# Performance work log

Hardware: AMD Instinct MI355X
Metric: run time of the kernel (lower is better)

The kernel has to match this reference:

```python
import jax, jax.numpy as jnp
import numpy as np

B, S, H, NH, HD = 2, 2048, 1024, 16, 64
RD = 16            # rotary_dim = head_dim * 0.25
W = 16             # mini_context_length (sliding window)
SCALE = HD ** -0.5
ROPE_BASE = 10000.0


def setup_inputs() -> dict:
    key = jax.random.key(0)
    ks = jax.random.split(key, 10)
    p = lambda k, shape: (jax.random.normal(k, shape, dtype=jnp.float32) * 0.02)
    return {
        "hidden_states": jax.random.normal(ks[0], (B, S, H), dtype=jnp.float32),
        "Wqkv": p(ks[1], (3 * H, H)), "bqkv": p(ks[2], (3 * H,)),
        "Wqa": p(ks[3], (H, H)),      "bqa": p(ks[4], (H,)),
        "Wka": p(ks[5], (H, H)),      "bka": p(ks[6], (H,)),
        "Wd": p(ks[7], (H, H)),       "bd": p(ks[8], (H,)),
    }


def _rotate_half(x):
    x1, x2 = jnp.split(x, 2, axis=-1)
    return jnp.concatenate([-x2, x1], axis=-1)


def _apply_rope(q, k, seq_len):
    # GPT-NeoX style rotary on the first RD dims. q,k: [B,NH,S,RD]
    inv_freq = 1.0 / (ROPE_BASE ** (jnp.arange(0, RD, 2, dtype=jnp.float32) / RD))
    t = jnp.arange(seq_len, dtype=jnp.float32)
    freqs = jnp.outer(t, inv_freq)                     # [S, RD//2]
    emb = jnp.concatenate([freqs, freqs], axis=-1)     # [S, RD]
    cos = jnp.cos(emb)[None, None]                      # [1,1,S,RD]
    sin = jnp.sin(emb)[None, None]
    return q * cos + _rotate_half(q) * sin, k * cos + _rotate_half(k) * sin


def reference(hidden_states, Wqkv, bqkv, Wqa, bqa, Wka, bka, Wd, bd):
    b, s, _ = hidden_states.shape
    qkv = hidden_states @ Wqkv.T + bqkv                       # [B,S,3H]
    qkv = qkv.reshape(b, s, 3, NH, HD).transpose(2, 0, 3, 1, 4)
    q, k, v = qkv[0], qkv[1], qkv[2]                          # [B,NH,S,HD]

    q_rot, k_rot = _apply_rope(q[..., :RD], k[..., :RD], s)
    q = jnp.concatenate([q_rot, q[..., RD:]], axis=-1)
    k = jnp.concatenate([k_rot, k[..., RD:]], axis=-1)

    # ----- Stage 1: sliding-window local attention (vectorized) -----
    pos = jnp.arange(s)
    idx = pos[:, None] - (W - 1) + jnp.arange(W)[None, :]     # [S,W]
    valid = idx >= 0
    idxc = jnp.clip(idx, 0, s - 1)
    k_win = k[:, :, idxc, :]                                   # [B,NH,S,W,HD]
    v_win = v[:, :, idxc, :]
    scores = jnp.einsum('bhsd,bhswd->bhsw', q, k_win) * SCALE
    scores = jnp.where(valid[None, None], scores, -jnp.inf)
    probs = jax.nn.softmax(scores, axis=-1)
    A = jnp.einsum('bhsw,bhswd->bhsd', probs, v_win)           # [B,NH,S,HD]

    A_hidden = A.transpose(0, 2, 1, 3).reshape(b, s, H)        # [B,S,H]

    # ----- Stage 2: causal global attention over A -----
    qa = (A_hidden @ Wqa.T + bqa).reshape(b, s, NH, HD).transpose(0, 2, 1, 3)
    ka = (A_hidden @ Wka.T + bka).reshape(b, s, NH, HD).transpose(0, 2, 1, 3)
    g = jnp.einsum('bhqd,bhkd->bhqk', qa, ka) * SCALE          # [B,NH,S,S]
    causal = pos[:, None] >= pos[None, :]
    g = jnp.where(causal[None, None], g, -jnp.inf)
    pg = jax.nn.softmax(g, axis=-1)
    out = jnp.einsum('bhqk,bhkd->bhqd', pg, A)                 # [B,NH,S,HD]
    out = out.transpose(0, 2, 1, 3).reshape(b, s, H)
    return out @ Wd.T + bd
```

## Files before the change

kernel.cpp:

```cpp
#include <hip/hip_runtime.h>
#include <hip/hip_bf16.h>
#include <cstdint>
#include <cstddef>

typedef __bf16 bf16;
typedef __bf16 bf16x4 __attribute__((ext_vector_type(4)));
typedef __bf16 bf16x8 __attribute__((ext_vector_type(8)));
typedef float  f32x4  __attribute__((ext_vector_type(4)));

#define DEVINL __device__ __forceinline__

constexpr int   Bc  = 2, Sc = 2048, Hc = 1024, NHc = 16, HDc = 64;
constexpr int   Tc  = Bc * Sc;
constexpr float L2E = 1.44269504088896340736f;
constexpr float NEG_BIG = -1.0e30f;

typedef __attribute__((address_space(1))) void AS1void;
typedef __attribute__((address_space(3))) void AS3void;

DEVINL void load_lds16(const bf16* g, bf16* l) {
  __builtin_amdgcn_global_load_lds((AS1void*)g, (AS3void*)l, 16, 0, 0);
}


__global__ __launch_bounds__(256)
void convert_all(const float* __restrict__ hs, const float* __restrict__ Wqkv,
                 const float* __restrict__ Wqa, const float* __restrict__ Wka,
                 const float* __restrict__ Wd, const float* __restrict__ bqa,
                 const float* __restrict__ bka,
                 bf16* __restrict__ hsb, bf16* __restrict__ wqkvb,
                 bf16* __restrict__ wqakab, bf16* __restrict__ wdb,
                 float* __restrict__ bqaka) {
  const int blk = blockIdx.x;
  if (blk >= 5120) {
    const int i = threadIdx.x * 8;
    const float* src = (i < 1024) ? (bqa + i) : (bka + i - 1024);
    *(f32x4*)(bqaka + i)     = *(const f32x4*)src;
    *(f32x4*)(bqaka + i + 4) = *(const f32x4*)(src + 4);
    return;
  }
  const float* src; bf16* dst; int base;
  if      (blk < 2048) { src = hs;   dst = hsb;                    base = blk; }
  else if (blk < 3584) { src = Wqkv; dst = wqkvb;                  base = blk - 2048; }
  else if (blk < 4096) { src = Wqa;  dst = wqakab;                 base = blk - 3584; }
  else if (blk < 4608) { src = Wka;  dst = wqakab + 1024 * 1024;   base = blk - 4096; }
  else                 { src = Wd;   dst = wdb;                    base = blk - 4608; }
  const int i = (base * 256 + threadIdx.x) * 8;
  f32x4 a = *(const f32x4*)(src + i);
  f32x4 b = *(const f32x4*)(src + i + 4);
  bf16x8 v;
#pragma unroll
  for (int j = 0; j < 4; j++) { v[j] = (bf16)a[j]; v[4 + j] = (bf16)b[j]; }
  *(bf16x8*)(dst + i) = v;
}

template <typename CT>
__global__ __launch_bounds__(256, 2)
void gemm128(const bf16* __restrict__ A, const bf16* __restrict__ Bw,
             const float* __restrict__ bias, CT* __restrict__ C,
             int M, int N, int K) {
  __shared__ __attribute__((aligned(16))) bf16 As[128 * 64];
  __shared__ __attribute__((aligned(16))) bf16 Bs[128 * 64];

  const int tid = threadIdx.x, wv = tid >> 6, lane = tid & 63;
  const int m0 = blockIdx.y * 128, n0 = blockIdx.x * 128;
  const int col = lane & 15, quad = lane >> 4;
  const int wrow = (wv >> 1) * 64, wcol = (wv & 1) * 64;

  f32x4 acc[4][4];
#pragma unroll
  for (int i = 0; i < 4; i++)
#pragma unroll
    for (int j = 0; j < 4; j++) acc[i][j] = f32x4{0.f, 0.f, 0.f, 0.f};

  const int srow = tid >> 3;
  const int scol = (((tid & 7) ^ (srow & 7)) << 3);
  const bf16* Ag = A  + (size_t)(m0 + srow) * K + scol;
  const bf16* Bg = Bw + (size_t)(n0 + srow) * K + scol;
  const int cs = col & 7;

  for (int k0 = 0; k0 < K; k0 += 64) {
#pragma unroll
    for (int c = 0; c < 4; c++) {
      load_lds16(Ag + (size_t)(c * 32) * K + k0, As + c * 2048 + tid * 8);
      load_lds16(Bg + (size_t)(c * 32) * K + k0, Bs + c * 2048 + tid * 8);
    }
    __syncthreads();
#pragma unroll
    for (int kk = 0; kk < 64; kk += 32) {
      const int so = ((((kk >> 3) + quad) ^ cs) << 3);
      bf16x8 af[4], bfr[4];
#pragma unroll
      for (int i = 0; i < 4; i++)
        af[i] = *(const bf16x8*)(As + (wrow + i * 16 + col) * 64 + so);
#pragma unroll
      for (int j = 0; j < 4; j++)
        bfr[j] = *(const bf16x8*)(Bs + (wcol + j * 16 + col) * 64 + so);
#pragma unroll
      for (int i = 0; i < 4; i++)
#pragma unroll
        for (int j = 0; j < 4; j++)
          acc[i][j] = __builtin_amdgcn_mfma_f32_16x16x32_bf16(af[i], bfr[j], acc[i][j], 0, 0, 0);
    }
    __syncthreads();
  }

#pragma unroll
  for (int j = 0; j < 4; j++) {
    const int c = n0 + wcol + j * 16 + col;
    const float bv = bias[c];
#pragma unroll
    for (int i = 0; i < 4; i++)
#pragma unroll
      for (int r = 0; r < 4; r++) {
        const int rr = m0 + wrow + i * 16 + quad * 4 + r;
        C[(size_t)rr * N + c] = (CT)(acc[i][j][r] + bv);
      }
  }
}

template <typename CT>
__global__ __launch_bounds__(256, 2)
void gemm64(const bf16* __restrict__ A, const bf16* __restrict__ Bw,
            const float* __restrict__ bias, CT* __restrict__ C,
            int M, int N, int K) {
  __shared__ __attribute__((aligned(16))) bf16 As[64 * 64];
  __shared__ __attribute__((aligned(16))) bf16 Bs[128 * 64];

  const int tid = threadIdx.x, wv = tid >> 6, lane = tid & 63;
  const int m0 = blockIdx.y * 64, n0 = blockIdx.x * 128;
  const int col = lane & 15, quad = lane >> 4;
  const int wrow = (wv >> 1) * 32, wcol = (wv & 1) * 64;

  f32x4 acc[2][4];
#pragma unroll
  for (int i = 0; i < 2; i++)
#pragma unroll
    for (int j = 0; j < 4; j++) acc[i][j] = f32x4{0.f, 0.f, 0.f, 0.f};

  const int srow = tid >> 3;
  const int scol = (((tid & 7) ^ (srow & 7)) << 3);
  const bf16* Ag = A  + (size_t)(m0 + srow) * K + scol;
  const bf16* Bg = Bw + (size_t)(n0 + srow) * K + scol;
  const int cs = col & 7;

  for (int k0 = 0; k0 < K; k0 += 64) {
#pragma unroll
    for (int c = 0; c < 2; c++)
      load_lds16(Ag + (size_t)(c * 32) * K + k0, As + c * 2048 + tid * 8);
#pragma unroll
    for (int c = 0; c < 4; c++)
      load_lds16(Bg + (size_t)(c * 32) * K + k0, Bs + c * 2048 + tid * 8);
    __syncthreads();
#pragma unroll
    for (int kk = 0; kk < 64; kk += 32) {
      const int so = ((((kk >> 3) + quad) ^ cs) << 3);
      bf16x8 af[2], bfr[4];
#pragma unroll
      for (int i = 0; i < 2; i++)
        af[i] = *(const bf16x8*)(As + (wrow + i * 16 + col) * 64 + so);
#pragma unroll
      for (int j = 0; j < 4; j++)
        bfr[j] = *(const bf16x8*)(Bs + (wcol + j * 16 + col) * 64 + so);
#pragma unroll
      for (int i = 0; i < 2; i++)
#pragma unroll
        for (int j = 0; j < 4; j++)
          acc[i][j] = __builtin_amdgcn_mfma_f32_16x16x32_bf16(af[i], bfr[j], acc[i][j], 0, 0, 0);
    }
    __syncthreads();
  }

#pragma unroll
  for (int j = 0; j < 4; j++) {
    const int c = n0 + wcol + j * 16 + col;
    const float bv = bias[c];
#pragma unroll
    for (int i = 0; i < 2; i++)
#pragma unroll
      for (int r = 0; r < 4; r++) {
        const int rr = m0 + wrow + i * 16 + quad * 4 + r;
        C[(size_t)rr * N + c] = (CT)(acc[i][j][r] + bv);
      }
  }
}

__global__ __launch_bounds__(256)
void window_attn(const bf16* __restrict__ qkv, bf16* __restrict__ Ah,
                 bf16* __restrict__ VTg) {
  __shared__ __attribute__((aligned(16))) bf16 Kw[31 * 72];
  __shared__ __attribute__((aligned(16))) bf16 Vw[31 * 72];
  const int g  = blockIdx.x;
  const int st = g & 127;
  const int h  = (g >> 7) & 15;
  const int b  = g >> 11;
  const int s0 = st * 16;
  const int tid = threadIdx.x;

  if ((tid < 124) || (tid >= 128 && tid < 252)) {
    const bool isK = tid < 124;
    const int lt  = isK ? tid : tid - 128;
    const int r   = lt >> 2, off = (lt & 3) << 4;
    int sidx = s0 - 15 + r; if (sidx < 0) sidx = 0;
    const bf16* src = qkv + (size_t)(b * Sc + sidx) * 3072 + (isK ? 1024 : 2048) + h * 64 + off;
    bf16x8 v0 = *(const bf16x8*)src;
    bf16x8 v1 = *(const bf16x8*)(src + 8);
    if (isK && off == 0) {
#pragma unroll
      for (int j = 0; j < 8; j++) {
        const float invf = exp2f(-(float)j * 1.66096404744368128f);
        float sn, csn;
        sincosf((float)sidx * invf, &sn, &csn);
        const float x1 = (float)v0[j], x2 = (float)v1[j];
        v0[j] = (bf16)(x1 * csn - x2 * sn);
        v1[j] = (bf16)(x2 * csn + x1 * sn);
      }
    }
    bf16* dst = (isK ? Kw : Vw) + r * 72 + off;
    *(bf16x8*)dst       = v0;
    *(bf16x8*)(dst + 8) = v1;
  }
  __syncthreads();

  const int wv = tid >> 6, lane = tid & 63;
  const int subq = lane >> 4, lane16 = lane & 15;
  const int s = s0 + wv * 4 + subq;
  const int t = b * Sc + s;
  const int d0 = lane16 * 4;

  float qd[4];
  {
    bf16x4 qv = *(const bf16x4*)(qkv + (size_t)t * 3072 + h * 64 + d0);
#pragma unroll
    for (int j = 0; j < 4; j++) qd[j] = (float)qv[j];
  }
  float pd[4];
#pragma unroll
  for (int j = 0; j < 4; j++) pd[j] = __shfl_xor(qd[j], 2, 64);
  if (lane16 < 4) {
#pragma unroll
    for (int j = 0; j < 4; j++) {
      const int jabs = d0 + j;
      const float invf = exp2f(-(float)(jabs & 7) * 1.66096404744368128f);
      float sn, csn;
      sincosf((float)s * invf, &sn, &csn);
      qd[j] = (jabs < 8) ? (qd[j] * csn - pd[j] * sn) : (qd[j] * csn + pd[j] * sn);
    }
  }

  float sc[16];
#pragma unroll
  for (int w = 0; w < 16; w++) {
    const int idxp = s - 15 + w;
    const int row = idxp - s0 + 15;
    bf16x4 kv = *(const bf16x4*)(Kw + row * 72 + d0);
    float p = qd[0] * (float)kv[0] + qd[1] * (float)kv[1] +
              qd[2] * (float)kv[2] + qd[3] * (float)kv[3];
#pragma unroll
    for (int m = 1; m < 16; m <<= 1) p += __shfl_xor(p, m, 64);
    sc[w] = (idxp < 0) ? NEG_BIG : p * 0.125f;
  }
  float mx = sc[0];
#pragma unroll
  for (int w = 1; w < 16; w++) mx = fmaxf(mx, sc[w]);
  float sum = 0.f;
#pragma unroll
  for (int w = 0; w < 16; w++) { sc[w] = exp2f((sc[w] - mx) * L2E); sum += sc[w]; }
  const float inv = 1.0f / fmaxf(sum, 1e-30f);

  float acc[4] = {0.f, 0.f, 0.f, 0.f};
#pragma unroll
  for (int w = 0; w < 16; w++) {
    const int idxp = s - 15 + w;
    const int row = idxp - s0 + 15;
    bf16x4 vv = *(const bf16x4*)(Vw + row * 72 + d0);
#pragma unroll
    for (int j = 0; j < 4; j++) acc[j] += sc[w] * (float)vv[j];
  }
  bf16x4 ov;
#pragma unroll
  for (int j = 0; j < 4; j++) ov[j] = (bf16)(acc[j] * inv);
  *(bf16x4*)(Ah + (size_t)t * 1024 + h * 64 + d0) = ov;
  bf16* vt = VTg + (((size_t)(b * 16 + h)) * 64 + d0) * 2048 + s;
#pragma unroll
  for (int j = 0; j < 4; j++) vt[(size_t)j * 2048] = ov[j];
}

__global__ __launch_bounds__(256, 2)
void flash_attn(const bf16* __restrict__ Q, const bf16* __restrict__ Kt,
                const bf16* __restrict__ VTg, bf16* __restrict__ O) {
  constexpr int QS = 2048;
  constexpr float SHIFT = 16.0f;
  __shared__ __attribute__((aligned(16))) bf16 K_lds[128 * 64];
  __shared__ __attribute__((aligned(16))) bf16 VT_lds[64 * 128];
  __shared__ __attribute__((aligned(16))) bf16 P_lds[4][16 * 136];

  const int tid = threadIdx.x, wv = tid >> 6, lane = tid & 63;
  const int bh = blockIdx.x;
  const int pr = blockIdx.y;
  const int b = bh >> 4, h = bh & 15;
  const int col = lane & 15, quad = lane >> 4;
  const size_t bS = (size_t)b * Sc;
  const int hd = h * 64;

  const int krow = tid >> 3;
  const int kcol = (((tid & 7) ^ (krow & 7)) << 3);
  const int vrow = tid >> 4;
  const int vcol = (((tid & 15) ^ vrow) << 3);
  const int cs8 = col & 7;

  for (int ph = 0; ph < 2; ph++) {
    const int qt = (ph == 0) ? pr : 31 - pr;
    const int qbase = qt * 64 + wv * 16;
    const int nkt = (qt + 2) >> 1;

    const bf16* qptr = Q + (bS + qbase + col) * QS + hd + quad * 8;
    bf16x8 qf[2];
    qf[0] = *(const bf16x8*)qptr;
    qf[1] = *(const bf16x8*)(qptr + 32);
#pragma unroll
    for (int hh = 0; hh < 2; hh++)
#pragma unroll
      for (int j = 0; j < 8; j++) qf[hh][j] = (bf16)((float)qf[hh][j] * 0.125f);

    f32x4 oacc[4];
#pragma unroll
    for (int i = 0; i < 4; i++) oacc[i] = f32x4{0.f, 0.f, 0.f, 0.f};
    float lrow[4] = {0.f, 0.f, 0.f, 0.f};

    for (int kt0 = 0; kt0 < nkt; kt0++) {
      const int k0 = kt0 * 128;
#pragma unroll
      for (int c = 0; c < 4; c++) {
        load_lds16(Kt + (bS + k0 + c * 32 + krow) * QS + hd + kcol,
                   K_lds + c * 2048 + tid * 8);
        load_lds16(VTg + ((size_t)bh * 64 + c * 16 + vrow) * 2048 + k0 + vcol,
                   VT_lds + c * 2048 + tid * 8);
      }
      __syncthreads();

      f32x4 sacc[8];
#pragma unroll
      for (int sub = 0; sub < 8; sub++) {
        f32x4 a = f32x4{0.f, 0.f, 0.f, 0.f};
#pragma unroll
        for (int hh = 0; hh < 2; hh++) {
          const int so = (((hh * 4 + quad) ^ cs8) << 3);
          bf16x8 kf = *(const bf16x8*)(K_lds + (sub * 16 + col) * 64 + so);
          a = __builtin_amdgcn_mfma_f32_16x16x32_bf16(qf[hh], kf, a, 0, 0, 0);
        }
        sacc[sub] = a;
      }
      if (kt0 == nkt - 1) {
#pragma unroll
        for (int sub = 0; sub < 8; sub++)
#pragma unroll
          for (int r = 0; r < 4; r++) {
            const int key = k0 + sub * 16 + col;
            const int qq  = qbase + quad * 4 + r;
            if (key > qq) sacc[sub][r] = NEG_BIG;
          }
      }
#pragma unroll
      for (int sub = 0; sub < 8; sub++)
#pragma unroll
        for (int r = 0; r < 4; r++)
          sacc[sub][r] = exp2f(sacc[sub][r] * L2E - SHIFT);
#pragma unroll
      for (int r = 0; r < 4; r++)
        lrow[r] += ((sacc[0][r] + sacc[1][r]) + (sacc[2][r] + sacc[3][r]))
                 + ((sacc[4][r] + sacc[5][r]) + (sacc[6][r] + sacc[7][r]));
#pragma unroll
      for (int sub = 0; sub < 8; sub++)
#pragma unroll
        for (int r = 0; r < 4; r++)
          P_lds[wv][(quad * 4 + r) * 136 + sub * 16 + col] = (bf16)sacc[sub][r];
#pragma unroll
      for (int kk = 0; kk < 128; kk += 32) {
        bf16x8 pf = *(const bf16x8*)&P_lds[wv][col * 136 + kk + quad * 8];
        const int vso = ((((kk >> 3) + quad) ^ col) << 3);
#pragma unroll
        for (int nb = 0; nb < 4; nb++) {
          bf16x8 vf = *(const bf16x8*)(VT_lds + (nb * 16 + col) * 128 + vso);
          oacc[nb] = __builtin_amdgcn_mfma_f32_16x16x32_bf16(pf, vf, oacc[nb], 0, 0, 0);
        }
      }
      __syncthreads();
    }

#pragma unroll
    for (int m = 1; m < 16; m <<= 1)
#pragma unroll
      for (int r = 0; r < 4; r++) lrow[r] += __shfl_xor(lrow[r], m, 64);
#pragma unroll
    for (int r = 0; r < 4; r++) lrow[r] = 1.0f / fmaxf(lrow[r], 1e-37f);
#pragma unroll
    for (int nb = 0; nb < 4; nb++)
#pragma unroll
      for (int r = 0; r < 4; r++) {
        const int qq = qbase + quad * 4 + r;
        O[(bS + qq) * 1024 + hd + nb * 16 + col] = (bf16)(oacc[nb][r] * lrow[r]);
      }
  }
}

extern "C" void kernel_launch(void* const* d_in, const int* in_sizes, int n_in,
                              void* d_out, int out_size, void* d_ws, size_t ws_size,
                              hipStream_t stream) {
  (void)in_sizes; (void)n_in; (void)out_size; (void)ws_size;
  const float* hs   = (const float*)d_in[0];
  const float* Wqkv = (const float*)d_in[1];
  const float* bqkv = (const float*)d_in[2];
  const float* Wqa  = (const float*)d_in[3];
  const float* bqa  = (const float*)d_in[4];
  const float* Wka  = (const float*)d_in[5];
  const float* bka  = (const float*)d_in[6];
  const float* Wd   = (const float*)d_in[7];
  const float* bd   = (const float*)d_in[8];
  float* out = (float*)d_out;

  const size_t TH = (size_t)Tc * Hc;
  bf16* dob   = (bf16*)d_out;
  bf16* hsb   = dob;
  bf16* wqkvb = dob + TH;
  bf16* Ah    = dob;
  bf16* VTg   = dob + TH;
  bf16* ws     = (bf16*)d_ws;
  bf16* qkv    = ws;
  bf16* qaka   = ws;
  bf16* oh     = ws + 2 * TH;
  bf16* wqakab = ws + 3 * TH;
  bf16* wdb    = wqakab + 2 * 1024 * 1024;
  float* bqaka = (float*)(wdb + 1024 * 1024);

  convert_all<<<dim3(5121), 256, 0, stream>>>(hs, Wqkv, Wqa, Wka, Wd, bqa, bka,
                                              hsb, wqkvb, wqakab, wdb, bqaka);

  gemm128<bf16><<<dim3(24, 32), 256, 0, stream>>>(hsb, wqkvb, bqkv, qkv, Tc, 3 * Hc, Hc);
  window_attn<<<dim3(Tc * NHc / 16), 256, 0, stream>>>(qkv, Ah, VTg);
  gemm128<bf16><<<dim3(16, 32), 256, 0, stream>>>(Ah, wqakab, bqaka, qaka, Tc, 2 * Hc, Hc);
  flash_attn<<<dim3(Bc * NHc, 16), 256, 0, stream>>>(qaka, qaka + Hc, VTg, oh);
  gemm64<float><<<dim3(8, 64), 256, 0, stream>>>(oh, wdb, bd, out, Tc, Hc, Hc);
}
```

Measured before the change: 234.2 us.

## Split flash-attn q-tile pairs into separate blocks, shrink output GEMM tile, raise occupancy

The flash attention kernel no longer loops over a paired short and long query tile inside one block. Each block now handles a single query tile, which doubles the grid to 32 tiles per head, and tiles are ordered in interleaved groups to spread causal work across the launch. The final projection GEMM moves to a 64x64 tile, giving twice as many blocks with one MFMA row per wave. Launch-bounds occupancy hints are raised on the GEMMs and flash kernel. The aim is better GPU fill and latency hiding, at the cost of less per-block work balancing, less data reuse in the smaller GEMM tile, and possible register pressure from the higher occupancy targets.

```diff
diff --git a/kernel.cpp b/kernel.cpp
--- a/kernel.cpp
+++ b/kernel.cpp
@@ -55,7 +55,7 @@
 }
 
 template <typename CT>
-__global__ __launch_bounds__(256, 2)
+__global__ __launch_bounds__(256, 3)
 void gemm128(const bf16* __restrict__ A, const bf16* __restrict__ Bw,
              const float* __restrict__ bias, CT* __restrict__ C,
              int M, int N, int K) {
@@ -120,23 +120,20 @@
 }
 
 template <typename CT>
-__global__ __launch_bounds__(256, 2)
-void gemm64(const bf16* __restrict__ A, const bf16* __restrict__ Bw,
-            const float* __restrict__ bias, CT* __restrict__ C,
-            int M, int N, int K) {
+__global__ __launch_bounds__(256, 4)
+void gemm6464(const bf16* __restrict__ A, const bf16* __restrict__ Bw,
+              const float* __restrict__ bias, CT* __restrict__ C,
+              int M, int N, int K) {
   __shared__ __attribute__((aligned(16))) bf16 As[64 * 64];
-  __shared__ __attribute__((aligned(16))) bf16 Bs[128 * 64];
+  __shared__ __attribute__((aligned(16))) bf16 Bs[64 * 64];
 
   const int tid = threadIdx.x, wv = tid >> 6, lane = tid & 63;
-  const int m0 = blockIdx.y * 64, n0 = blockIdx.x * 128;
+  const int m0 = blockIdx.y * 64, n0 = blockIdx.x * 64;
   const int col = lane & 15, quad = lane >> 4;
-  const int wrow = (wv >> 1) * 32, wcol = (wv & 1) * 64;
-
-  f32x4 acc[2][4];
-#pragma unroll
-  for (int i = 0; i < 2; i++)
-#pragma unroll
-    for (int j = 0; j < 4; j++) acc[i][j] = f32x4{0.f, 0.f, 0.f, 0.f};
+
+  f32x4 acc[4];
+#pragma unroll
+  for (int j = 0; j < 4; j++) acc[j] = f32x4{0.f, 0.f, 0.f, 0.f};
 
   const int srow = tid >> 3;
   const int scol = (((tid & 7) ^ (srow & 7)) << 3);
@@ -146,42 +143,33 @@
 
   for (int k0 = 0; k0 < K; k0 += 64) {
 #pragma unroll
-    for (int c = 0; c < 2; c++)
+    for (int c = 0; c < 2; c++) {
       load_lds16(Ag + (size_t)(c * 32) * K + k0, As + c * 2048 + tid * 8);
-#pragma unroll
-    for (int c = 0; c < 4; c++)
       load_lds16(Bg + (size_t)(c * 32) * K + k0, Bs + c * 2048 + tid * 8);
+    }
     __syncthreads();
 #pragma unroll
     for (int kk = 0; kk < 64; kk += 32) {
       const int so = ((((kk >> 3) + quad) ^ cs) << 3);
-      bf16x8 af[2], bfr[4];
-#pragma unroll
-      for (int i = 0; i < 2; i++)
-        af[i] = *(const bf16x8*)(As + (wrow + i * 16 + col) * 64 + so);
-#pragma unroll
-      for (int j = 0; j < 4; j++)
-        bfr[j] = *(const bf16x8*)(Bs + (wcol + j * 16 + col) * 64 + so);
-#pragma unroll
-      for (int i = 0; i < 2; i++)
-#pragma unroll
-        for (int j = 0; j < 4; j++)
-          acc[i][j] = __builtin_amdgcn_mfma_f32_16x16x32_bf16(af[i], bfr[j], acc[i][j], 0, 0, 0);
+      bf16x8 af = *(const bf16x8*)(As + (wv * 16 + col) * 64 + so);
+#pragma unroll
+      for (int j = 0; j < 4; j++) {
+        bf16x8 bfr = *(const bf16x8*)(Bs + (j * 16 + col) * 64 + so);
+        acc[j] = __builtin_amdgcn_mfma_f32_16x16x32_bf16(af, bfr, acc[j], 0, 0, 0);
+      }
     }
     __syncthreads();
   }
 
 #pragma unroll
   for (int j = 0; j < 4; j++) {
-    const int c = n0 + wcol + j * 16 + col;
+    const int c = n0 + j * 16 + col;
     const float bv = bias[c];
 #pragma unroll
-    for (int i = 0; i < 2; i++)
-#pragma unroll
-      for (int r = 0; r < 4; r++) {
-        const int rr = m0 + wrow + i * 16 + quad * 4 + r;
-        C[(size_t)rr * N + c] = (CT)(acc[i][j][r] + bv);
-      }
+    for (int r = 0; r < 4; r++) {
+      const int rr = m0 + wv * 16 + quad * 4 + r;
+      C[(size_t)rr * N + c] = (CT)(acc[j][r] + bv);
+    }
   }
 }
 
@@ -286,7 +274,7 @@
   for (int j = 0; j < 4; j++) vt[(size_t)j * 2048] = ov[j];
 }
 
-__global__ __launch_bounds__(256, 2)
+__global__ __launch_bounds__(256, 3)
 void flash_attn(const bf16* __restrict__ Q, const bf16* __restrict__ Kt,
                 const bf16* __restrict__ VTg, bf16* __restrict__ O) {
   constexpr int QS = 2048;
@@ -297,7 +285,10 @@
 
   const int tid = threadIdx.x, wv = tid >> 6, lane = tid & 63;
   const int bh = blockIdx.x;
-  const int pr = blockIdx.y;
+  const int y  = blockIdx.y;
+  const int gq = y & 7, kq = y >> 3;
+  const int qt = (kq == 0) ? gq : (kq == 1) ? (15 - gq)
+               : (kq == 2) ? (16 + gq) : (31 - gq);
   const int b = bh >> 4, h = bh & 15;
   const int col = lane & 15, quad = lane >> 4;
   const size_t bS = (size_t)b * Sc;
@@ -309,99 +300,96 @@
   const int vcol = (((tid & 15) ^ vrow) << 3);
   const int cs8 = col & 7;
 
-  for (int ph = 0; ph < 2; ph++) {
-    const int qt = (ph == 0) ? pr : 31 - pr;
-    const int qbase = qt * 64 + wv * 16;
-    const int nkt = (qt + 2) >> 1;
-
-    const bf16* qptr = Q + (bS + qbase + col) * QS + hd + quad * 8;
-    bf16x8 qf[2];
-    qf[0] = *(const bf16x8*)qptr;
-    qf[1] = *(const bf16x8*)(qptr + 32);
-#pragma unroll
-    for (int hh = 0; hh < 2; hh++)
-#pragma unroll
-      for (int j = 0; j < 8; j++) qf[hh][j] = (bf16)((float)qf[hh][j] * 0.125f);
-
-    f32x4 oacc[4];
-#pragma unroll
-    for (int i = 0; i < 4; i++) oacc[i] = f32x4{0.f, 0.f, 0.f, 0.f};
-    float lrow[4] = {0.f, 0.f, 0.f, 0.f};
-
-    for (int kt0 = 0; kt0 < nkt; kt0++) {
-      const int k0 = kt0 * 128;
-#pragma unroll
-      for (int c = 0; c < 4; c++) {
-        load_lds16(Kt + (bS + k0 + c * 32 + krow) * QS + hd + kcol,
-                   K_lds + c * 2048 + tid * 8);
-        load_lds16(VTg + ((size_t)bh * 64 + c * 16 + vrow) * 2048 + k0 + vcol,
-                   VT_lds + c * 2048 + tid * 8);
+  const int qbase = qt * 64 + wv * 16;
+  const int nkt = (qt + 2) >> 1;
+
+  const bf16* qptr = Q + (bS + qbase + col) * QS + hd + quad * 8;
+  bf16x8 qf[2];
+  qf[0] = *(const bf16x8*)qptr;
+  qf[1] = *(const bf16x8*)(qptr + 32);
+#pragma unroll
+  for (int hh = 0; hh < 2; hh++)
+#pragma unroll
+    for (int j = 0; j < 8; j++) qf[hh][j] = (bf16)((float)qf[hh][j] * 0.125f);
+
+  f32x4 oacc[4];
+#pragma unroll
+  for (int i = 0; i < 4; i++) oacc[i] = f32x4{0.f, 0.f, 0.f, 0.f};
+  float lrow[4] = {0.f, 0.f, 0.f, 0.f};
+
+  for (int kt0 = 0; kt0 < nkt; kt0++) {
+    const int k0 = kt0 * 128;
+#pragma unroll
+    for (int c = 0; c < 4; c++) {
+      load_lds16(Kt + (bS + k0 + c * 32 + krow) * QS + hd + kcol,
+                 K_lds + c * 2048 + tid * 8);
+      load_lds16(VTg + ((size_t)bh * 64 + c * 16 + vrow) * 2048 + k0 + vcol,
+                 VT_lds + c * 2048 + tid * 8);
+    }
+    __syncthreads();
+
+    f32x4 sacc[8];
+#pragma unroll
+    for (int sub = 0; sub < 8; sub++) {
+      f32x4 a = f32x4{0.f, 0.f, 0.f, 0.f};
+#pragma unroll
+      for (int hh = 0; hh < 2; hh++) {
+        const int so = (((hh * 4 + quad) ^ cs8) << 3);
+        bf16x8 kf = *(const bf16x8*)(K_lds + (sub * 16 + col) * 64 + so);
+        a = __builtin_amdgcn_mfma_f32_16x16x32_bf16(qf[hh], kf, a, 0, 0, 0);
       }
-      __syncthreads();
-
-      f32x4 sacc[8];
-#pragma unroll
-      for (int sub = 0; sub < 8; sub++) {
-        f32x4 a = f32x4{0.f, 0.f, 0.f, 0.f};
-#pragma unroll
-        for (int hh = 0; hh < 2; hh++) {
-          const int so = (((hh * 4 + quad) ^ cs8) << 3);
-          bf16x8 kf = *(const bf16x8*)(K_lds + (sub * 16 + col) * 64 + so);
-          a = __builtin_amdgcn_mfma_f32_16x16x32_bf16(qf[hh], kf, a, 0, 0, 0);
+      sacc[sub] = a;
+    }
+    if (kt0 == nkt - 1) {
+#pragma unroll
+      for (int sub = 0; sub < 8; sub++)
+#pragma unroll
+        for (int r = 0; r < 4; r++) {
+          const int key = k0 + sub * 16 + col;
+          const int qq  = qbase + quad * 4 + r;
+          if (key > qq) sacc[sub][r] = NEG_BIG;
         }
-        sacc[sub] = a;
+    }
+#pragma unroll
+    for (int sub = 0; sub < 8; sub++)
+#pragma unroll
+      for (int r = 0; r < 4; r++)
+        sacc[sub][r] = exp2f(sacc[sub][r] * L2E - SHIFT);
+#pragma unroll
+    for (int r = 0; r < 4; r++)
+      lrow[r] += ((sacc[0][r] + sacc[1][r]) + (sacc[2][r] + sacc[3][r]))
+               + ((sacc[4][r] + sacc[5][r]) + (sacc[6][r] + sacc[7][r]));
+#pragma unroll
+    for (int sub = 0; sub < 8; sub++)
+#pragma unroll
+      for (int r = 0; r < 4; r++)
+        P_lds[wv][(quad * 4 + r) * 136 + sub * 16 + col] = (bf16)sacc[sub][r];
+#pragma unroll
+    for (int kk = 0; kk < 128; kk += 32) {
+      bf16x8 pf = *(const bf16x8*)&P_lds[wv][col * 136 + kk + quad * 8];
+      const int vso = ((((kk >> 3) + quad) ^ col) << 3);
+#pragma unroll
+      for (int nb = 0; nb < 4; nb++) {
+        bf16x8 vf = *(const bf16x8*)(VT_lds + (nb * 16 + col) * 128 + vso);
+        oacc[nb] = __builtin_amdgcn_mfma_f32_16x16x32_bf16(pf, vf, oacc[nb], 0, 0, 0);
       }
-      if (kt0 == nkt - 1) {
-#pragma unroll
-        for (int sub = 0; sub < 8; sub++)
-#pragma unroll
-          for (int r = 0; r < 4; r++) {
-            const int key = k0 + sub * 16 + col;
-            const int qq  = qbase + quad * 4 + r;
-            if (key > qq) sacc[sub][r] = NEG_BIG;
-          }
-      }
-#pragma unroll
-      for (int sub = 0; sub < 8; sub++)
-#pragma unroll
-        for (int r = 0; r < 4; r++)
-          sacc[sub][r] = exp2f(sacc[sub][r] * L2E - SHIFT);
-#pragma unroll
-      for (int r = 0; r < 4; r++)
-        lrow[r] += ((sacc[0][r] + sacc[1][r]) + (sacc[2][r] + sacc[3][r]))
-                 + ((sacc[4][r] + sacc[5][r]) + (sacc[6][r] + sacc[7][r]));
-#pragma unroll
-      for (int sub = 0; sub < 8; sub++)
-#pragma unroll
-        for (int r = 0; r < 4; r++)
-          P_lds[wv][(quad * 4 + r) * 136 + sub * 16 + col] = (bf16)sacc[sub][r];
-#pragma unroll
-      for (int kk = 0; kk < 128; kk += 32) {
-        bf16x8 pf = *(const bf16x8*)&P_lds[wv][col * 136 + kk + quad * 8];
-        const int vso = ((((kk >> 3) + quad) ^ col) << 3);
-#pragma unroll
-        for (int nb = 0; nb < 4; nb++) {
-          bf16x8 vf = *(const bf16x8*)(VT_lds + (nb * 16 + col) * 128 + vso);
-          oacc[nb] = __builtin_amdgcn_mfma_f32_16x16x32_bf16(pf, vf, oacc[nb], 0, 0, 0);
-        }
-      }
-      __syncthreads();
-    }
-
-#pragma unroll
-    for (int m = 1; m < 16; m <<= 1)
-#pragma unroll
-      for (int r = 0; r < 4; r++) lrow[r] += __shfl_xor(lrow[r], m, 64);
-#pragma unroll
-    for (int r = 0; r < 4; r++) lrow[r] = 1.0f / fmaxf(lrow[r], 1e-37f);
-#pragma unroll
-    for (int nb = 0; nb < 4; nb++)
-#pragma unroll
-      for (int r = 0; r < 4; r++) {
-        const int qq = qbase + quad * 4 + r;
-        O[(bS + qq) * 1024 + hd + nb * 16 + col] = (bf16)(oacc[nb][r] * lrow[r]);
-      }
-  }
+    }
+    __syncthreads();
+  }
+
+#pragma unroll
+  for (int m = 1; m < 16; m <<= 1)
+#pragma unroll
+    for (int r = 0; r < 4; r++) lrow[r] += __shfl_xor(lrow[r], m, 64);
+#pragma unroll
+  for (int r = 0; r < 4; r++) lrow[r] = 1.0f / fmaxf(lrow[r], 1e-37f);
+#pragma unroll
+  for (int nb = 0; nb < 4; nb++)
+#pragma unroll
+    for (int r = 0; r < 4; r++) {
+      const int qq = qbase + quad * 4 + r;
+      O[(bS + qq) * 1024 + hd + nb * 16 + col] = (bf16)(oacc[nb][r] * lrow[r]);
+    }
 }
 
 extern "C" void kernel_launch(void* const* d_in, const int* in_sizes, int n_in,
@@ -439,6 +427,6 @@
   gemm128<bf16><<<dim3(24, 32), 256, 0, stream>>>(hsb, wqkvb, bqkv, qkv, Tc, 3 * Hc, Hc);
   window_attn<<<dim3(Tc * NHc / 16), 256, 0, stream>>>(qkv, Ah, VTg);
   gemm128<bf16><<<dim3(16, 32), 256, 0, stream>>>(Ah, wqakab, bqaka, qaka, Tc, 2 * Hc, Hc);
-  flash_attn<<<dim3(Bc * NHc, 16), 256, 0, stream>>>(qaka, qaka + Hc, VTg, oh);
-  gemm64<float><<<dim3(8, 64), 256, 0, stream>>>(oh, wdb, bd, out, Tc, Hc, Hc);
-}
+  flash_attn<<<dim3(Bc * NHc, 32), 256, 0, stream>>>(qaka, qaka + Hc, VTg, oh);
+  gemm6464<float><<<dim3(16, 64), 256, 0, stream>>>(oh, wdb, bd, out, Tc, Hc, Hc);
+}
```

Measured after the change: 232.8 us. No clear change (-0.6%).
